# Optimization experiments

Measured on AMD Instinct MI355X. Metric: run time of the kernel, lower is better.

Reference implementation:

```python
import jax, jax.numpy as jnp
import numpy as np

N_R, N_U, N_P = 40000, 30000, 30000
N = N_R + N_U + N_P
E = 1600000
NFEAT, NHID, NCLASS = 128, 128, 40


def setup_inputs() -> dict:
    key = jax.random.key(0)
    ks = jax.random.split(key, 12)
    s = 0.05
    return {
        "inputx_r": jax.random.normal(ks[0], (N_R, 5), jnp.float32),
        "inputx_u": jax.random.normal(ks[1], (N_U, 7), jnp.float32),
        "inputx_p": jax.random.normal(ks[2], (N_P, 6), jnp.float32),
        "edge_index": jax.random.randint(ks[3], (2, E), 0, N, jnp.int64)
            if jax.config.jax_enable_x64 else jax.random.randint(ks[3], (2, E), 0, N, jnp.int32),
        "W_r": jax.random.normal(ks[4], (5, NFEAT), jnp.float32) * s,
        "b_r": jax.random.normal(ks[5], (NFEAT,), jnp.float32) * s,
        "W_u": jax.random.normal(ks[6], (7, NFEAT), jnp.float32) * s,
        "b_u": jax.random.normal(ks[7], (NFEAT,), jnp.float32) * s,
        "W_p": jax.random.normal(ks[8], (6, NFEAT), jnp.float32) * s,
        "b_p": jax.random.normal(ks[9], (NFEAT,), jnp.float32) * s,
        "W1": jax.random.normal(ks[10], (NFEAT, NHID), jnp.float32) * s,
        "W2": jax.random.normal(ks[11], (NHID, NCLASS), jnp.float32) * s,
    }


def _gcn_conv(x, W, src, dst, num_nodes):
    # GCNConv(add_self_loops=False, normalize=False, bias=False):
    # out = A @ (x @ W), unit edge weights, aggregation at dst of source messages.
    h = x @ W                                      # [N, d_out]
    return jax.ops.segment_sum(h[src], dst, num_segments=num_nodes)


def reference(inputx_r, inputx_u, inputx_p, edge_index,
              W_r, b_r, W_u, b_u, W_p, b_p, W1, W2):
    # Segment-wise input projections (nums = [[N_R, N_R+N_U], [.,.], [.,.]]
    # with empty 2nd/3rd blocks; tail is the p-segment), then two GCN layers.
    x = jnp.concatenate([
        inputx_r @ W_r + b_r,   # nodes [0 : N_R]
        inputx_u @ W_u + b_u,   # nodes [N_R : N_R+N_U]
        inputx_p @ W_p + b_p,   # nodes [N_R+N_U : N]
    ], axis=0)                  # [N, NFEAT]
    src, dst = edge_index[0], edge_index[1]
    h = jax.nn.relu(_gcn_conv(x, W1, src, dst, N))   # gc1 + relu
    # dropout: inference (training=False) -> identity
    out = _gcn_conv(h, W2, src, dst, N)              # gc2
    return out
```

## Files before the change

### kernel.cpp

```cpp
#include <hip/hip_runtime.h>

constexpr int kNR = 40000;
constexpr int kNU = 30000;
constexpr int kNP = 30000;
constexpr int kN  = 100000;
constexpr int kE  = 1600000;
constexpr int kF  = 128;
constexpr int kC  = 40;
constexpr int kBN = 64;
constexpr int kNB = (kN + kBN - 1) / kBN;
constexpr int kNBp = 1600;
constexpr int kSlot = 2048;
constexpr int kPackB = 98;
constexpr int kFuseB = kPackB;
constexpr int kW2B   = kPackB + 1;
constexpr int kScat0 = kPackB + 2;
constexpr int kScatB = 128;
constexpr int kCE    = kE / kScatB;
constexpr int kPrepB = kScat0 + kScatB;

typedef __attribute__((ext_vector_type(8))) short bf16x8;
typedef __attribute__((ext_vector_type(4))) float f32x4;

__device__ __forceinline__ float bf_to_f(unsigned short h) {
    union { unsigned int i; float f; } u; u.i = ((unsigned int)h) << 16; return u.f;
}
__device__ __forceinline__ unsigned short f_to_bf(float f) {
    union { unsigned int i; float f; } u; u.f = f;
    unsigned int r = u.i + 0x7FFFu + ((u.i >> 16) & 1u);
    return (unsigned short)(r >> 16);
}
__device__ __forceinline__ float2 bf2_to_f2(unsigned int p) {
    union { unsigned int i; float f; } lo, hi;
    lo.i = (p & 0xFFFFu) << 16;
    hi.i = p & 0xFFFF0000u;
    return make_float2(lo.f, hi.f);
}
__device__ __forceinline__ unsigned int pack_bf2(float a, float b) {
    return (unsigned int)f_to_bf(a) | ((unsigned int)f_to_bf(b) << 16);
}
__device__ __forceinline__ float ldf(const void* p, int i, int isbf) {
    return isbf ? bf_to_f(((const unsigned short*)p)[i]) : ((const float*)p)[i];
}
__device__ __forceinline__ int lde(const int* p, int i, int is64) {
    return is64 ? p[2 * i] : p[i];
}

__device__ __forceinline__ int sniff_isbf(const void* W1, int t, int* sh) {
    if (t < 64) {
        unsigned int wv = ((const unsigned int*)W1)[t];
        unsigned int ax = wv & 0x7FFFu;
        int pl = (ax == 0u) || (ax > 0x2000u && ax < 0x4000u);
        unsigned long long mk = __ballot(pl);
        if (t == 0) *sh = (__popcll(mk) >= 48) ? 1 : 0;
    }
    __syncthreads();
    return *sh;
}

__global__ void __launch_bounds__(1024) gcn_prep(
        const void* __restrict__ xr, const void* __restrict__ xu, const void* __restrict__ xp,
        const void* __restrict__ Wr, const void* __restrict__ br,
        const void* __restrict__ Wu, const void* __restrict__ bu,
        const void* __restrict__ Wp, const void* __restrict__ bp,
        const void* __restrict__ W1, const void* __restrict__ W2,
        const int* __restrict__ ei,
        unsigned short* __restrict__ fwfrag, unsigned short* __restrict__ w2frag,
        uint4* __restrict__ xpack, int* __restrict__ gcnt,
        unsigned int* __restrict__ slots) {
    __shared__ __align__(16) char smem[29696];
    __shared__ int sflag;
    int t = threadIdx.x;
    int bx = blockIdx.x;
    if (bx < kPackB) {
        int isbf = sniff_isbf(W1, t, &sflag);
        int n = bx * 1024 + t;
        if (n >= kN) return;
        const void* base; int roff, d;
        if (n < kNR)            { base = xr; roff = n * 5;               d = 5; }
        else if (n < kNR + kNU) { base = xu; roff = (n - kNR) * 7;       d = 7; }
        else                    { base = xp; roff = (n - kNR - kNU) * 6; d = 6; }
        float f[8];
        #pragma unroll
        for (int i = 0; i < 8; i++) f[i] = (i < d) ? ldf(base, roff + i, isbf) : 0.f;
        uint4 u;
        u.x = pack_bf2(f[0], f[1]);  u.y = pack_bf2(f[2], f[3]);
        u.z = pack_bf2(f[4], f[5]);  u.w = pack_bf2(f[6], f[7]);
        xpack[n] = u;
    } else if (bx == kFuseB) {
        int isbf = sniff_isbf(W1, t, &sflag);
        float* sw   = (float*)smem;
        float* pacc = (float*)(smem + 10752);
        unsigned short* flds = (unsigned short*)(smem + 21504);
        for (int i = t; i < 21 * kF; i += 1024) {
            int r = i >> 7, c = i & 127;
            float v;
            if (r < 5)        v = ldf(Wr, r * kF + c, isbf);
            else if (r < 12)  v = ldf(Wu, (r - 5) * kF + c, isbf);
            else if (r < 18)  v = ldf(Wp, (r - 12) * kF + c, isbf);
            else if (r == 18) v = ldf(br, c, isbf);
            else if (r == 19) v = ldf(bu, c, isbf);
            else              v = ldf(bp, c, isbf);
            sw[i] = v;
        }
        __syncthreads();
        {
            bool active = (t < 256);
            int j = t & 127, half = (t >> 7) & 1;
            float acc[21];
            #pragma unroll
            for (int r = 0; r < 21; r++) acc[r] = 0.f;
            if (active) {
                int k0 = half * 64, k1 = k0 + 64;
                for (int k = k0; k < k1; k++) {
                    float w1 = ldf(W1, k * kF + j, isbf);
                    #pragma unroll
                    for (int r = 0; r < 21; r++) acc[r] += sw[r * kF + k] * w1;
                }
            }
            if (active && half == 1) {
                #pragma unroll
                for (int r = 0; r < 21; r++) pacc[r * kF + j] = acc[r];
            }
            __syncthreads();
            if (active && half == 0) {
                #pragma unroll
                for (int r = 0; r < 21; r++) acc[r] += pacc[r * kF + j];
                unsigned short row[32];
                #pragma unroll
                for (int s = 0; s < 32; s++) row[s] = 0;
                #pragma unroll
                for (int i = 0; i < 5; i++) row[0  + i] = f_to_bf(acc[i]);
                #pragma unroll
                for (int i = 0; i < 7; i++) row[8  + i] = f_to_bf(acc[5 + i]);
                #pragma unroll
                for (int i = 0; i < 6; i++) row[16 + i] = f_to_bf(acc[12 + i]);
                row[24] = f_to_bf(acc[18]);  row[25] = f_to_bf(acc[19]);  row[26] = f_to_bf(acc[20]);
                #pragma unroll
                for (int s = 0; s < 32; s++) flds[j * 32 + s] = row[s];
            }
        }
        __syncthreads();
        for (int idx = t; idx < 8 * 64; idx += 1024) {
            int t8 = idx >> 6, lane = idx & 63;
            int mm = lane & 15, q = lane >> 4;
            #pragma unroll
            for (int j = 0; j < 8; j++)
                fwfrag[idx * 8 + j] = flds[(16 * t8 + mm) * 32 + q * 8 + j];
        }
    } else if (bx == kW2B) {
        int isbf = sniff_isbf(W1, t, &sflag);
        for (int idx = t; idx < 12 * 64; idx += 1024) {
            int st = idx >> 6, lane = idx & 63;
            int s = st / 3, tt = st % 3;
            int mm = lane & 15, q = lane >> 4;
            int cls = 16 * tt + mm;
            #pragma unroll
            for (int j = 0; j < 8; j++) {
                int k = s * 32 + q * 8 + j;
                w2frag[idx * 8 + j] = (cls < kC) ? f_to_bf(ldf(W2, k * kC + cls, isbf))
                                                 : (unsigned short)0;
            }
        }
    } else {
        int* hist = (int*)smem;
        int* cur  = (int*)(smem + 6400);
        if (t < 64) {
            int v = ((const int*)ei)[2 * t + 1];
            unsigned long long mk = __ballot(v != 0);
            if (t == 0) sflag = (mk == 0ull) ? 1 : 0;
        }
        for (int i = t; i < kNBp; i += 1024) hist[i] = 0;
        __syncthreads();
        int is64 = sflag;
        int blk = bx - kScat0;
        int e0 = blk * kCE, e1 = e0 + kCE;
        for (int eb = e0 + t; eb < e1; eb += 4096) {
            unsigned int d[4];
            #pragma unroll
            for (int j = 0; j < 4; j++) {
                int e = eb + j * 1024;
                d[j] = (e < e1) ? (unsigned int)lde(ei, kE + e, is64) : 0xFFFFFFFFu;
            }
            #pragma unroll
            for (int j = 0; j < 4; j++)
                if (d[j] < (unsigned int)kN) atomicAdd(&hist[d[j] >> 6], 1);
        }
        __syncthreads();
        int off = (blk * 401) % kNBp;
        for (int j = t; j < kNBp; j += 1024) {
            int i = j + off;
            if (i >= kNBp) i -= kNBp;
            int h = hist[i];
            cur[i] = (h > 0) ? atomicAdd(&gcnt[i], h) : 0;
        }
        __syncthreads();
        for (int eb = e0 + t; eb < e1; eb += 4096) {
            unsigned int d[4], s[4];
            #pragma unroll
            for (int j = 0; j < 4; j++) {
                int e = eb + j * 1024;
                d[j] = (e < e1) ? (unsigned int)lde(ei, kE + e, is64) : 0xFFFFFFFFu;
            }
            #pragma unroll
            for (int j = 0; j < 4; j++) {
                int e = eb + j * 1024;
                s[j] = (e < e1) ? (unsigned int)lde(ei, e, is64) : 0u;
            }
            #pragma unroll
            for (int j = 0; j < 4; j++) {
                if (d[j] < (unsigned int)kN) {
                    unsigned int sv = (s[j] < (unsigned int)kN) ? s[j] : 0u;
                    int b = (int)(d[j] >> 6);
                    int pos = atomicAdd(&cur[b], 1);
                    if (pos < kSlot) slots[(size_t)b * kSlot + pos] = (sv << 6) | (d[j] & 63u);
                }
            }
        }
    }
}

__global__ void __launch_bounds__(256) GCN_2190433321521_kernel(
        const unsigned int* __restrict__ slots,
        const int* __restrict__ gcnt,
        const uint4* __restrict__ xpack,
        const unsigned short* __restrict__ fwfrag,
        const unsigned short* __restrict__ w2frag,
        int* __restrict__ rpb,
        int* __restrict__ rpe,
        int* __restrict__ col,
        unsigned short* __restrict__ hw) {
    __shared__ __align__(16) char smem[25600];
    float*          agg_l  = (float*)smem;
    int*            cnt_l  = (int*)(smem + 7424);
    int*            strt_l = (int*)(smem + 7680);
    int*            cntv_l = (int*)(smem + 7936);
    unsigned int*   wst    = (unsigned int*)(smem + 8192);
    int*            col_l  = (int*)(smem + 16384);
    unsigned short* hbuf   = (unsigned short*)(smem + 8192);
    unsigned short* cst    = (unsigned short*)smem;

    int b = blockIdx.x;
    int base = b * kBN;
    int nn = min(kBN, kN - base);
    int tid = threadIdx.x;

    if (tid < kBN) cnt_l[tid] = 0;
    __syncthreads();
    int p0 = b * kSlot;
    int m = min(gcnt[b], kSlot);
    int p1 = p0 + m;

    for (int ib = p0 + tid; ib < p1; ib += 1024) {
        unsigned int w[4]; int ok[4];
        #pragma unroll
        for (int j = 0; j < 4; j++) {
            int i = ib + j * 256;
            ok[j] = (i < p1);
            w[j] = ok[j] ? slots[i] : 0u;
        }
        #pragma unroll
        for (int j = 0; j < 4; j++) {
            int i = ib + j * 256;
            if (ok[j]) {
                wst[i - p0] = w[j];
                atomicAdd(&cnt_l[w[j] & 63u], 1);
            }
        }
    }
    __syncthreads();
    if (tid < 64) {
        int v = cnt_l[tid];
        int incl = v;
        #pragma unroll
        for (int o = 1; o < 64; o <<= 1) {
            int y = __shfl_up(incl, o, 64);
            if (tid >= o) incl += y;
        }
        int cursor = p0 + incl - v;
        cnt_l[tid]  = cursor;
        strt_l[tid] = cursor;
        cntv_l[tid] = v;
        if (tid < nn) { rpb[base + tid] = cursor; rpe[base + tid] = cursor + v; }
    }
    __syncthreads();

    for (int i = p0 + tid; i < p1; i += 256) {
        unsigned int w = wst[i - p0];
        unsigned int s = w >> 6;
        int dloc = (int)(w & 63u);
        int pos = atomicAdd(&cnt_l[dloc], 1);
        col_l[pos - p0] = (int)s;
    }
    __syncthreads();
    for (int i = tid; i < m; i += 256) col[p0 + i] = col_l[i];

    {
        int node = tid >> 2, j = tid & 3;
        float aR[8], aU[8], aP[8];
        #pragma unroll
        for (int i = 0; i < 8; i++) { aR[i] = 0.f; aU[i] = 0.f; aP[i] = 0.f; }
        float cR = 0.f, cU = 0.f, cP = 0.f;
        int start = strt_l[node] - p0;
        int c = cntv_l[node];
        for (int i = start + j; i < start + c; i += 4) {
            int s = col_l[i];
            uint4 u = xpack[s];
            float2 q0 = bf2_to_f2(u.x), q1 = bf2_to_f2(u.y);
            float2 q2 = bf2_to_f2(u.z), q3 = bf2_to_f2(u.w);
            if (s < kNR) {
                aR[0]+=q0.x; aR[1]+=q0.y; aR[2]+=q1.x; aR[3]+=q1.y;
                aR[4]+=q2.x; aR[5]+=q2.y; aR[6]+=q3.x; aR[7]+=q3.y; cR += 1.f;
            } else if (s < kNR + kNU) {
                aU[0]+=q0.x; aU[1]+=q0.y; aU[2]+=q1.x; aU[3]+=q1.y;
                aU[4]+=q2.x; aU[5]+=q2.y; aU[6]+=q3.x; aU[7]+=q3.y; cU += 1.f;
            } else {
                aP[0]+=q0.x; aP[1]+=q0.y; aP[2]+=q1.x; aP[3]+=q1.y;
                aP[4]+=q2.x; aP[5]+=q2.y; aP[6]+=q3.x; aP[7]+=q3.y; cP += 1.f;
            }
        }
        #pragma unroll
        for (int i = 0; i < 8; i++) {
            float v = aR[i];
            v += __shfl_xor(v, 1, 64);  v += __shfl_xor(v, 2, 64);
            if (j == 0) agg_l[node * 29 + i] = v;
        }
        #pragma unroll
        for (int i = 0; i < 8; i++) {
            float v = aU[i];
            v += __shfl_xor(v, 1, 64);  v += __shfl_xor(v, 2, 64);
            if (j == 0) agg_l[node * 29 + 8 + i] = v;
        }
        #pragma unroll
        for (int i = 0; i < 8; i++) {
            float v = aP[i];
            v += __shfl_xor(v, 1, 64);  v += __shfl_xor(v, 2, 64);
            if (j == 0) agg_l[node * 29 + 16 + i] = v;
        }
        float v = cR;
        v += __shfl_xor(v, 1, 64);  v += __shfl_xor(v, 2, 64);
        if (j == 0) agg_l[node * 29 + 24] = v;
        v = cU;
        v += __shfl_xor(v, 1, 64);  v += __shfl_xor(v, 2, 64);
        if (j == 0) agg_l[node * 29 + 25] = v;
        v = cP;
        v += __shfl_xor(v, 1, 64);  v += __shfl_xor(v, 2, 64);
        if (j == 0) agg_l[node * 29 + 26] = v;
    }
    __syncthreads();

    int wid = tid >> 6, lane = tid & 63;
    int mm = lane & 15, q = lane >> 4;
    int node = wid * 16 + mm;
    bf16x8 a1;
    #pragma unroll
    for (int j = 0; j < 8; j++) {
        int sl = q * 8 + j;
        a1[j] = (sl < 27) ? (short)f_to_bf(agg_l[node * 29 + sl]) : (short)0;
    }
    __syncthreads();
    const bf16x8* fwf = (const bf16x8*)fwfrag;
    f32x4 c1[8];
    #pragma unroll
    for (int t = 0; t < 8; t++) {
        f32x4 z = {0.f, 0.f, 0.f, 0.f};
        c1[t] = __builtin_amdgcn_mfma_f32_16x16x32_bf16(a1, fwf[t * 64 + lane], z, 0, 0, 0);
    }
    unsigned short* hb = hbuf + wid * 16 * 136;
    #pragma unroll
    for (int t = 0; t < 8; t++) {
        #pragma unroll
        for (int r = 0; r < 4; r++)
            hb[(q * 4 + r) * 136 + 16 * t + mm] = f_to_bf(fmaxf(c1[t][r], 0.f));
    }
    const bf16x8* w2f = (const bf16x8*)w2frag;
    f32x4 c2[3];
    #pragma unroll
    for (int t = 0; t < 3; t++) { c2[t].x = 0.f; c2[t].y = 0.f; c2[t].z = 0.f; c2[t].w = 0.f; }
    #pragma unroll
    for (int s = 0; s < 4; s++) {
        bf16x8 a2 = *(const bf16x8*)&hb[mm * 136 + s * 32 + q * 8];
        #pragma unroll
        for (int t = 0; t < 3; t++)
            c2[t] = __builtin_amdgcn_mfma_f32_16x16x32_bf16(a2, w2f[(s * 3 + t) * 64 + lane],
                                                            c2[t], 0, 0, 0);
    }
    #pragma unroll
    for (int t = 0; t < 3; t++) {
        int cls = 16 * t + mm;
        if (cls < kC) {
            #pragma unroll
            for (int r = 0; r < 4; r++)
                cst[(wid * 16 + q * 4 + r) * kC + cls] = f_to_bf(c2[t][r]);
        }
    }
    __syncthreads();
    {
        int tot = nn * (kC / 2);
        const unsigned int* cs32 = (const unsigned int*)cst;
        unsigned int* ho = (unsigned int*)(hw + (size_t)base * kC);
        for (int i = tid; i < tot; i += 256) ho[i] = cs32[i];
    }
}

__global__ void __launch_bounds__(256) gcn_gather2(const unsigned int* __restrict__ hw32,
                                                   const int* __restrict__ rpb,
                                                   const int* __restrict__ rpe,
                                                   const int* __restrict__ col,
                                                   unsigned int* __restrict__ out,
                                                   const void* __restrict__ W1) {
    __shared__ int sisbf;
    int t = threadIdx.x;
    int isbf = sniff_isbf(W1, t, &sisbf);
    int w = (blockIdx.x * 256 + t) >> 6;
    if (w >= kN) return;
    int lane = t & 63;
    int grp = lane / 10;
    int cp  = lane % 10;
    int beg = rpb[w], end = rpe[w];
    float f0 = 0.f, f1 = 0.f, f2 = 0.f, f3 = 0.f;
    if (grp < 6) {
        const uint2* hp = (const uint2*)hw32;
        int e = beg + grp;
        int c0 = (e      < end) ? col[e]      : -1;
        int c1 = (e + 6  < end) ? col[e + 6]  : -1;
        int c2 = (e + 12 < end) ? col[e + 12] : -1;
        int c3 = (e + 18 < end) ? col[e + 18] : -1;
        if (c0 >= 0) {
            uint2 v = hp[c0 * 10 + cp];
            float2 a = bf2_to_f2(v.x), bb = bf2_to_f2(v.y);
            f0 += a.x; f1 += a.y; f2 += bb.x; f3 += bb.y;
        }
        if (c1 >= 0) {
            uint2 v = hp[c1 * 10 + cp];
            float2 a = bf2_to_f2(v.x), bb = bf2_to_f2(v.y);
            f0 += a.x; f1 += a.y; f2 += bb.x; f3 += bb.y;
        }
        if (c2 >= 0) {
            uint2 v = hp[c2 * 10 + cp];
            float2 a = bf2_to_f2(v.x), bb = bf2_to_f2(v.y);
            f0 += a.x; f1 += a.y; f2 += bb.x; f3 += bb.y;
        }
        if (c3 >= 0) {
            uint2 v = hp[c3 * 10 + cp];
            float2 a = bf2_to_f2(v.x), bb = bf2_to_f2(v.y);
            f0 += a.x; f1 += a.y; f2 += bb.x; f3 += bb.y;
        }
        for (e += 24; e < end; e += 6) {
            int s = col[e];
            uint2 v = hp[s * 10 + cp];
            float2 a = bf2_to_f2(v.x), bb = bf2_to_f2(v.y);
            f0 += a.x; f1 += a.y; f2 += bb.x; f3 += bb.y;
        }
    }
    f0 += __shfl(f0, lane + 30, 64);
    f1 += __shfl(f1, lane + 30, 64);
    f2 += __shfl(f2, lane + 30, 64);
    f3 += __shfl(f3, lane + 30, 64);
    f0 += __shfl(f0, lane + 10, 64) + __shfl(f0, lane + 20, 64);
    f1 += __shfl(f1, lane + 10, 64) + __shfl(f1, lane + 20, 64);
    f2 += __shfl(f2, lane + 10, 64) + __shfl(f2, lane + 20, 64);
    f3 += __shfl(f3, lane + 10, 64) + __shfl(f3, lane + 20, 64);
    if (lane < 10) {
        if (isbf) {
            out[w * 20 + 2 * lane]     = pack_bf2(f0, f1);
            out[w * 20 + 2 * lane + 1] = pack_bf2(f2, f3);
        } else {
            float* of = (float*)out;
            of[w * 40 + 4 * lane]     = f0;
            of[w * 40 + 4 * lane + 1] = f1;
            of[w * 40 + 4 * lane + 2] = f2;
            of[w * 40 + 4 * lane + 3] = f3;
        }
    }
}

extern "C" void kernel_launch(void* const* d_in, const int* in_sizes, int n_in,
                              void* d_out, int out_size, void* d_ws, size_t ws_size,
                              hipStream_t stream) {
    const void* xr = d_in[0];
    const void* xu = d_in[1];
    const void* xp = d_in[2];
    const int*  ei = (const int*)d_in[3];
    const void* Wr = d_in[4];
    const void* br = d_in[5];
    const void* Wu = d_in[6];
    const void* bu = d_in[7];
    const void* Wp = d_in[8];
    const void* bp = d_in[9];
    const void* W1 = d_in[10];
    const void* W2 = d_in[11];
    (void)in_sizes; (void)n_in; (void)out_size; (void)ws_size;

    char* ws = (char*)d_ws;
    size_t off = 0;
    auto alloc = [&](size_t bytes) -> void* {
        void* p = (void*)(ws + off);
        off = (off + bytes + 255) & ~(size_t)255;
        return p;
    };
    int*            gcnt   = (int*)           alloc((size_t)kNBp * 4);
    unsigned short* fwfrag = (unsigned short*)alloc(8 * 64 * 8 * 2);
    unsigned short* w2frag = (unsigned short*)alloc(12 * 64 * 8 * 2);
    uint4*          xpack  = (uint4*)         alloc((size_t)kN * 16);
    unsigned int*   slots  = (unsigned int*)  alloc((size_t)kNB * kSlot * 4);
    int*            col    = (int*)           alloc((size_t)kNB * kSlot * 4);
    int*            rpb    = (int*)           alloc((size_t)kN * 4);
    int*            rpe    = (int*)           alloc((size_t)kN * 4);
    unsigned short* hwb    = (unsigned short*)alloc((size_t)kN * kC * 2);

    hipMemsetAsync(gcnt, 0, (size_t)kNBp * 4, stream);
    gcn_prep<<<kPrepB, 1024, 0, stream>>>(xr, xu, xp, Wr, br, Wu, bu, Wp, bp, W1, W2,
                                          ei, fwfrag, w2frag, xpack, gcnt, slots);
    GCN_2190433321521_kernel<<<kNB, 256, 0, stream>>>(slots, gcnt, xpack, fwfrag, w2frag,
                                                      rpb, rpe, col, hwb);
    gcn_gather2<<<(kN * 64 + 255) / 256, 256, 0, stream>>>((const unsigned int*)hwb, rpb, rpe,
                                                           col, (unsigned int*)d_out, W1);
}
```

Measured before the change: 176.7 us.

## Replace bucketed CSR build with per-node fixed-capacity neighbor slots

Edges are scattered directly into per-destination-node slot lists of fixed capacity 64, using global atomics on per-node counters. This replaces the per-64-node bucket histogram, the in-kernel prefix scan and the col/rowptr CSR construction. Both gather stages now read neighbors straight from the node's slot row, which removes a whole sort phase and its LDS traffic. The cost is 1.6M returning global atomics, scattered 4-byte writes, a larger slot buffer and a larger memset. Any node with in-degree above 64 silently loses edges.

```diff
diff --git a/kernel.cpp b/kernel.cpp
--- a/kernel.cpp
+++ b/kernel.cpp
@@ -9,13 +9,12 @@
 constexpr int kC  = 40;
 constexpr int kBN = 64;
 constexpr int kNB = (kN + kBN - 1) / kBN;
-constexpr int kNBp = 1600;
-constexpr int kSlot = 2048;
+constexpr int kNSlot = 64;
 constexpr int kPackB = 98;
 constexpr int kFuseB = kPackB;
 constexpr int kW2B   = kPackB + 1;
 constexpr int kScat0 = kPackB + 2;
-constexpr int kScatB = 128;
+constexpr int kScatB = 256;
 constexpr int kCE    = kE / kScatB;
 constexpr int kPrepB = kScat0 + kScatB;
 
@@ -67,7 +66,7 @@
         const int* __restrict__ ei,
         unsigned short* __restrict__ fwfrag, unsigned short* __restrict__ w2frag,
         uint4* __restrict__ xpack, int* __restrict__ gcnt,
-        unsigned int* __restrict__ slots) {
+        unsigned int* __restrict__ nslots) {
     __shared__ __align__(16) char smem[29696];
     __shared__ int sflag;
     int t = threadIdx.x;
@@ -163,46 +162,23 @@
             }
         }
     } else {
-        int* hist = (int*)smem;
-        int* cur  = (int*)(smem + 6400);
         if (t < 64) {
             int v = ((const int*)ei)[2 * t + 1];
             unsigned long long mk = __ballot(v != 0);
             if (t == 0) sflag = (mk == 0ull) ? 1 : 0;
         }
-        for (int i = t; i < kNBp; i += 1024) hist[i] = 0;
         __syncthreads();
         int is64 = sflag;
         int blk = bx - kScat0;
         int e0 = blk * kCE, e1 = e0 + kCE;
         for (int eb = e0 + t; eb < e1; eb += 4096) {
-            unsigned int d[4];
+            unsigned int d[4], s[4];
             #pragma unroll
             for (int j = 0; j < 4; j++) {
                 int e = eb + j * 1024;
                 d[j] = (e < e1) ? (unsigned int)lde(ei, kE + e, is64) : 0xFFFFFFFFu;
             }
             #pragma unroll
-            for (int j = 0; j < 4; j++)
-                if (d[j] < (unsigned int)kN) atomicAdd(&hist[d[j] >> 6], 1);
-        }
-        __syncthreads();
-        int off = (blk * 401) % kNBp;
-        for (int j = t; j < kNBp; j += 1024) {
-            int i = j + off;
-            if (i >= kNBp) i -= kNBp;
-            int h = hist[i];
-            cur[i] = (h > 0) ? atomicAdd(&gcnt[i], h) : 0;
-        }
-        __syncthreads();
-        for (int eb = e0 + t; eb < e1; eb += 4096) {
-            unsigned int d[4], s[4];
-            #pragma unroll
-            for (int j = 0; j < 4; j++) {
-                int e = eb + j * 1024;
-                d[j] = (e < e1) ? (unsigned int)lde(ei, kE + e, is64) : 0xFFFFFFFFu;
-            }
-            #pragma unroll
             for (int j = 0; j < 4; j++) {
                 int e = eb + j * 1024;
                 s[j] = (e < e1) ? (unsigned int)lde(ei, e, is64) : 0u;
@@ -211,9 +187,8 @@
             for (int j = 0; j < 4; j++) {
                 if (d[j] < (unsigned int)kN) {
                     unsigned int sv = (s[j] < (unsigned int)kN) ? s[j] : 0u;
-                    int b = (int)(d[j] >> 6);
-                    int pos = atomicAdd(&cur[b], 1);
-                    if (pos < kSlot) slots[(size_t)b * kSlot + pos] = (sv << 6) | (d[j] & 63u);
+                    int pos = atomicAdd(&gcnt[d[j]], 1);
+                    if (pos < kNSlot) nslots[(size_t)d[j] * kNSlot + pos] = sv;
                 }
             }
         }
@@ -221,23 +196,16 @@
 }
 
 __global__ void __launch_bounds__(256) GCN_2190433321521_kernel(
-        const unsigned int* __restrict__ slots,
+        const unsigned int* __restrict__ nslots,
         const int* __restrict__ gcnt,
         const uint4* __restrict__ xpack,
         const unsigned short* __restrict__ fwfrag,
         const unsigned short* __restrict__ w2frag,
-        int* __restrict__ rpb,
-        int* __restrict__ rpe,
-        int* __restrict__ col,
         unsigned short* __restrict__ hw) {
-    __shared__ __align__(16) char smem[25600];
+    __shared__ __align__(16) char smem[25088];
     float*          agg_l  = (float*)smem;
-    int*            cnt_l  = (int*)(smem + 7424);
-    int*            strt_l = (int*)(smem + 7680);
-    int*            cntv_l = (int*)(smem + 7936);
-    unsigned int*   wst    = (unsigned int*)(smem + 8192);
-    int*            col_l  = (int*)(smem + 16384);
-    unsigned short* hbuf   = (unsigned short*)(smem + 8192);
+    int*            deg_l  = (int*)(smem + 7424);
+    unsigned short* hbuf   = (unsigned short*)(smem + 7680);
     unsigned short* cst    = (unsigned short*)smem;
 
     int b = blockIdx.x;
@@ -245,55 +213,11 @@
     int nn = min(kBN, kN - base);
     int tid = threadIdx.x;
 
-    if (tid < kBN) cnt_l[tid] = 0;
+    if (tid < kBN) {
+        int n = base + tid;
+        deg_l[tid] = (n < kN) ? min(gcnt[n], kNSlot) : 0;
+    }
     __syncthreads();
-    int p0 = b * kSlot;
-    int m = min(gcnt[b], kSlot);
-    int p1 = p0 + m;
-
-    for (int ib = p0 + tid; ib < p1; ib += 1024) {
-        unsigned int w[4]; int ok[4];
-        #pragma unroll
-        for (int j = 0; j < 4; j++) {
-            int i = ib + j * 256;
-            ok[j] = (i < p1);
-            w[j] = ok[j] ? slots[i] : 0u;
-        }
-        #pragma unroll
-        for (int j = 0; j < 4; j++) {
-            int i = ib + j * 256;
-            if (ok[j]) {
-                wst[i - p0] = w[j];
-                atomicAdd(&cnt_l[w[j] & 63u], 1);
-            }
-        }
-    }
-    __syncthreads();
-    if (tid < 64) {
-        int v = cnt_l[tid];
-        int incl = v;
-        #pragma unroll
-        for (int o = 1; o < 64; o <<= 1) {
-            int y = __shfl_up(incl, o, 64);
-            if (tid >= o) incl += y;
-        }
-        int cursor = p0 + incl - v;
-        cnt_l[tid]  = cursor;
-        strt_l[tid] = cursor;
-        cntv_l[tid] = v;
-        if (tid < nn) { rpb[base + tid] = cursor; rpe[base + tid] = cursor + v; }
-    }
-    __syncthreads();
-
-    for (int i = p0 + tid; i < p1; i += 256) {
-        unsigned int w = wst[i - p0];
-        unsigned int s = w >> 6;
-        int dloc = (int)(w & 63u);
-        int pos = atomicAdd(&cnt_l[dloc], 1);
-        col_l[pos - p0] = (int)s;
-    }
-    __syncthreads();
-    for (int i = tid; i < m; i += 256) col[p0 + i] = col_l[i];
 
     {
         int node = tid >> 2, j = tid & 3;
@@ -301,10 +225,10 @@
         #pragma unroll
         for (int i = 0; i < 8; i++) { aR[i] = 0.f; aU[i] = 0.f; aP[i] = 0.f; }
         float cR = 0.f, cU = 0.f, cP = 0.f;
-        int start = strt_l[node] - p0;
-        int c = cntv_l[node];
-        for (int i = start + j; i < start + c; i += 4) {
-            int s = col_l[i];
+        int c = deg_l[node];
+        const unsigned int* nsl = nslots + (size_t)(base + node) * kNSlot;
+        for (int i = j; i < c; i += 4) {
+            int s = (int)nsl[i];
             uint4 u = xpack[s];
             float2 q0 = bf2_to_f2(u.x), q1 = bf2_to_f2(u.y);
             float2 q2 = bf2_to_f2(u.z), q3 = bf2_to_f2(u.w);
@@ -404,9 +328,8 @@
 }
 
 __global__ void __launch_bounds__(256) gcn_gather2(const unsigned int* __restrict__ hw32,
-                                                   const int* __restrict__ rpb,
-                                                   const int* __restrict__ rpe,
-                                                   const int* __restrict__ col,
+                                                   const int* __restrict__ gcnt,
+                                                   const unsigned int* __restrict__ nslots,
                                                    unsigned int* __restrict__ out,
                                                    const void* __restrict__ W1) {
     __shared__ int sisbf;
@@ -417,15 +340,16 @@
     int lane = t & 63;
     int grp = lane / 10;
     int cp  = lane % 10;
-    int beg = rpb[w], end = rpe[w];
+    int deg = min(gcnt[w], kNSlot);
+    const unsigned int* nsl = nslots + (size_t)w * kNSlot;
     float f0 = 0.f, f1 = 0.f, f2 = 0.f, f3 = 0.f;
     if (grp < 6) {
         const uint2* hp = (const uint2*)hw32;
-        int e = beg + grp;
-        int c0 = (e      < end) ? col[e]      : -1;
-        int c1 = (e + 6  < end) ? col[e + 6]  : -1;
-        int c2 = (e + 12 < end) ? col[e + 12] : -1;
-        int c3 = (e + 18 < end) ? col[e + 18] : -1;
+        int e = grp;
+        int c0 = (e      < deg) ? (int)nsl[e]      : -1;
+        int c1 = (e + 6  < deg) ? (int)nsl[e + 6]  : -1;
+        int c2 = (e + 12 < deg) ? (int)nsl[e + 12] : -1;
+        int c3 = (e + 18 < deg) ? (int)nsl[e + 18] : -1;
         if (c0 >= 0) {
             uint2 v = hp[c0 * 10 + cp];
             float2 a = bf2_to_f2(v.x), bb = bf2_to_f2(v.y);
@@ -446,8 +370,8 @@
             float2 a = bf2_to_f2(v.x), bb = bf2_to_f2(v.y);
             f0 += a.x; f1 += a.y; f2 += bb.x; f3 += bb.y;
         }
-        for (e += 24; e < end; e += 6) {
-            int s = col[e];
+        for (e += 24; e < deg; e += 6) {
+            int s = (int)nsl[e];
             uint2 v = hp[s * 10 + cp];
             float2 a = bf2_to_f2(v.x), bb = bf2_to_f2(v.y);
             f0 += a.x; f1 += a.y; f2 += bb.x; f3 += bb.y;
@@ -499,21 +423,17 @@
         off = (off + bytes + 255) & ~(size_t)255;
         return p;
     };
-    int*            gcnt   = (int*)           alloc((size_t)kNBp * 4);
+    int*            gcnt   = (int*)           alloc((size_t)kN * 4);
     unsigned short* fwfrag = (unsigned short*)alloc(8 * 64 * 8 * 2);
     unsigned short* w2frag = (unsigned short*)alloc(12 * 64 * 8 * 2);
     uint4*          xpack  = (uint4*)         alloc((size_t)kN * 16);
-    unsigned int*   slots  = (unsigned int*)  alloc((size_t)kNB * kSlot * 4);
-    int*            col    = (int*)           alloc((size_t)kNB * kSlot * 4);
-    int*            rpb    = (int*)           alloc((size_t)kN * 4);
-    int*            rpe    = (int*)           alloc((size_t)kN * 4);
+    unsigned int*   nslots = (unsigned int*)  alloc((size_t)kN * kNSlot * 4);
     unsigned short* hwb    = (unsigned short*)alloc((size_t)kN * kC * 2);
 
-    hipMemsetAsync(gcnt, 0, (size_t)kNBp * 4, stream);
+    hipMemsetAsync(gcnt, 0, (size_t)kN * 4, stream);
     gcn_prep<<<kPrepB, 1024, 0, stream>>>(xr, xu, xp, Wr, br, Wu, bu, Wp, bp, W1, W2,
-                                          ei, fwfrag, w2frag, xpack, gcnt, slots);
-    GCN_2190433321521_kernel<<<kNB, 256, 0, stream>>>(slots, gcnt, xpack, fwfrag, w2frag,
-                                                      rpb, rpe, col, hwb);
-    gcn_gather2<<<(kN * 64 + 255) / 256, 256, 0, stream>>>((const unsigned int*)hwb, rpb, rpe,
-                                                           col, (unsigned int*)d_out, W1);
-}
+                                          ei, fwfrag, w2frag, xpack, gcnt, nslots);
+    GCN_2190433321521_kernel<<<kNB, 256, 0, stream>>>(nslots, gcnt, xpack, fwfrag, w2frag, hwb);
+    gcn_gather2<<<(kN * 64 + 255) / 256, 256, 0, stream>>>((const unsigned int*)hwb, gcnt,
+                                                           nslots, (unsigned int*)d_out, W1);
+}
```

Result: slower. 304.0 us (+72.1%).
